# Kernel tuning notes

Measured on AMD Instinct MI355X. Metric: run time of the kernel, lower is better.

The kernel has to match this reference:

```python
import jax, jax.numpy as jnp
import numpy as np

H, FH, D = 8, 4, 64          # num_heads, focal_heads, att_size
HID = H * D                   # hidden_size = 512
B, S = 8, 512                 # batch, num_nodes
T_HOP, T_EDGE = 32, 16
SCALE = D ** -0.5


def setup_inputs() -> dict:
    key = jax.random.key(0)
    ks = jax.random.split(key, 24)
    f = lambda i, shape: jax.random.normal(ks[i], shape, jnp.float32)
    w = 1.0 / np.sqrt(HID)
    inp = {
        'q': f(0, (B, S, HID)), 'k': f(1, (B, S, HID)), 'v': f(2, (B, S, HID)),
        'query_hop_emb': f(3, (T_HOP, HID)) * 0.02,
        'query_edge_emb': f(4, (T_EDGE, HID)) * 0.02,
        'key_hop_emb': f(5, (T_HOP, HID)) * 0.02,
        'key_edge_emb': f(6, (T_EDGE, HID)) * 0.02,
        'value_hop_emb': f(7, (T_HOP, HID)) * 0.02,
        'value_edge_emb': f(8, (T_EDGE, HID)) * 0.02,
        'distance': jax.random.randint(ks[9], (B, S, S), 0, T_HOP),
        'edge_attr': jax.random.randint(ks[10], (B, S, S), 0, T_EDGE),
        # guarantee at least one unmasked key per query row to keep softmax finite
        'mask': jax.random.bernoulli(ks[11], 0.9, (B, S)).at[:, 0].set(True),
        'focal_mask': jax.random.bernoulli(ks[12], 0.5, (B, S, S)).at[:, :, 0].set(True),
        'Wq': f(13, (HID, H * D)) * w, 'bq': f(14, (H * D,)) * 0.01,
        'Wk': f(15, (HID, H * D)) * w, 'bk': f(16, (H * D,)) * 0.01,
        'Wv': f(17, (HID, H * D)) * w, 'bv': f(18, (H * D,)) * 0.01,
        'Wo': f(19, (H * D, HID)) * w, 'bo': f(20, (HID,)) * 0.01,
    }
    return inp


def _emb_scores(x, emb):
    # x: [B,H,S,D], emb: [T, H*D] -> per-head scores [B,H,S,T]
    e = emb.reshape(-1, H, D).transpose(1, 0, 2)  # [H,T,D]
    return jnp.einsum('bhsd,htd->bhst', x, e)


def _gather_last(scores, idx):
    # scores: [B,H,S,T], idx: [B,S,S] -> [B,H,S,S]
    idx_b = jnp.broadcast_to(idx[:, None], (B, H, S, S))
    return jnp.take_along_axis(scores, idx_b, axis=3)


def _scatter_add_last(attn, idx, T):
    # attn: [B,H,S,S], idx: [B,S,S] -> [B,H,S,T] accumulating attn weights
    idx_b = jnp.broadcast_to(idx[:, None], (B, H, S, S)).reshape(B * H * S, S)
    rows = jnp.arange(B * H * S)[:, None]
    flat = (rows * T + idx_b).reshape(-1)
    out = jnp.zeros((B * H * S * T,), attn.dtype).at[flat].add(attn.reshape(-1))
    return out.reshape(B, H, S, T)


def reference(q, k, v, query_hop_emb, query_edge_emb, key_hop_emb, key_edge_emb,
              value_hop_emb, value_edge_emb, distance, edge_attr, mask, focal_mask,
              Wq, bq, Wk, bk, Wv, bv, Wo, bo):
    qh = (q @ Wq + bq).reshape(B, S, H, D).transpose(0, 2, 1, 3)  # [B,H,S,D]
    kh = (k @ Wk + bk).reshape(B, S, H, D).transpose(0, 2, 1, 3)
    vh = (v @ Wv + bv).reshape(B, S, H, D).transpose(0, 2, 1, 3)

    spatial_bias = (_gather_last(_emb_scores(qh, query_hop_emb), distance)
                    + _gather_last(_emb_scores(kh, key_hop_emb), distance))
    edge_bias = (_gather_last(_emb_scores(qh, query_edge_emb), edge_attr)
                 + _gather_last(_emb_scores(kh, key_edge_emb), edge_attr))

    attn = (jnp.einsum('bhsd,bhtd->bhst', qh, kh) + spatial_bias + edge_bias) * SCALE

    GS = H - FH
    a1 = jnp.where(mask[:, None, None, :], attn[:, :GS], -jnp.inf)
    a2 = jnp.where(focal_mask[:, None], attn[:, GS:], -jnp.inf)
    attn = jax.nn.softmax(jnp.concatenate([a1, a2], axis=1), axis=3)

    vha = _scatter_add_last(attn, distance, T_HOP)   # [B,H,S,T_HOP]
    vea = _scatter_add_last(attn, edge_attr, T_EDGE)  # [B,H,S,T_EDGE]
    vh_emb = value_hop_emb.reshape(T_HOP, H, D).transpose(1, 0, 2)   # [H,T,D]
    ve_emb = value_edge_emb.reshape(T_EDGE, H, D).transpose(1, 0, 2)

    x = (jnp.einsum('bhst,bhtd->bhsd', attn, vh)
         + jnp.einsum('bhst,htd->bhsd', vha, vh_emb)
         + jnp.einsum('bhst,htd->bhsd', vea, ve_emb))
    x = x.transpose(0, 2, 1, 3).reshape(B, S, H * D)
    return x @ Wo + bo
```

## Files before the change

### kernel.cpp

```cpp
#include <hip/hip_runtime.h>

constexpr int nB = 8, nS = 512, nH = 8, nD = 64, nHID = 512;
constexpr int THOP = 32, TEDGE = 16;
constexpr float SCALE = 0.125f;
constexpr float NEGINF = -30000.0f;

typedef __attribute__((ext_vector_type(8))) short bf16x8;
typedef __attribute__((ext_vector_type(4))) float f32x4;

#define MFMA16(A, B, C) __builtin_amdgcn_mfma_f32_16x16x32_bf16(A, B, C, 0, 0, 0)

__device__ __align__(16) unsigned short g_qhi[(size_t)nB * nH * nS * nD];
__device__ __align__(16) unsigned short g_qlo[(size_t)nB * nH * nS * nD];
__device__ __align__(16) unsigned short g_khi[(size_t)nB * nH * nS * nD];
__device__ __align__(16) unsigned short g_klo[(size_t)nB * nH * nS * nD];
__device__ __align__(16) unsigned short g_vhiT[(size_t)nB * nH * nD * nS];
__device__ __align__(16) unsigned short g_vloT[(size_t)nB * nH * nD * nS];
__device__ __align__(16) unsigned short g_embh[96 * 512];
__device__ __align__(16) unsigned short g_embl[96 * 512];
__device__ __align__(16) unsigned short g_inhi[(size_t)3 * 2097152];
__device__ __align__(16) unsigned short g_inlo[(size_t)3 * 2097152];
__device__ __align__(16) unsigned short g_wth[(size_t)4 * 262144];
__device__ __align__(16) unsigned short g_wtl[(size_t)4 * 262144];
__device__ __align__(16) unsigned short g_xhi[(size_t)nB * nS * nHID];
__device__ __align__(16) unsigned short g_xlo[(size_t)nB * nS * nHID];
__device__ int g_flags[32];

__device__ __forceinline__ float ldf(const void* p, int isf32, size_t i) {
  if (isf32) return ((const float*)p)[i];
  unsigned int w = (unsigned int)(((const unsigned short*)p)[i]) << 16;
  return __uint_as_float(w);
}
__device__ __forceinline__ float bf2f(unsigned short h) {
  return __uint_as_float((unsigned)h << 16);
}
__device__ __forceinline__ float4 ldf4(const void* p, int isf32, size_t i) {
  if (isf32) return ((const float4*)p)[i >> 2];
  const ushort4 u = ((const ushort4*)p)[i >> 2];
  float4 r;
  r.x = bf2f(u.x); r.y = bf2f(u.y); r.z = bf2f(u.z); r.w = bf2f(u.w);
  return r;
}
__device__ __forceinline__ unsigned short f2bf(float x) {
  unsigned u = __float_as_uint(x);
  u += 0x7FFFu + ((u >> 16) & 1u);
  return (unsigned short)(u >> 16);
}

__device__ int detect_bool_mode(const unsigned char* p) {
  if (p[0] == 0x80 && p[1] == 0x3F) return 2;
  if (p[0] == 0x00 && p[1] == 0x3C) return 4;
  if (p[0] == 0x00 && p[3] == 0x3F) return 3;
  for (int i = 0; i < 64; i += 4)
    if (p[i + 1] | p[i + 2] | p[i + 3]) return 1;
  return 0;
}
__device__ __forceinline__ bool bool_at(const unsigned char* p, int mode, size_t i) {
  switch (mode) {
    case 0: return ((const int*)p)[i] != 0;
    case 1: return p[i] != 0;
    case 3: return ((const float*)p)[i] != 0.f;
    default: return ((const unsigned short*)p)[i] != 0;
  }
}

__global__ __launch_bounds__(256) void detect_all(
    const void* q, const void* k, const void* v,
    const void* qhe, const void* qee, const void* khe, const void* kee,
    const void* vhe, const void* vee,
    const int* dist, const int* edge,
    const unsigned char* mraw, const unsigned char* fraw,
    const void* Wq, const void* bq, const void* Wk, const void* bk,
    const void* Wv, const void* bv, const void* Wo, const void* bo) {
  __shared__ float sred[256];
  __shared__ int nzs;
  const int tid = threadIdx.x;
  const int blk = blockIdx.x;

  if (blk < 17) {
    const void* arrs[17] = {q, k, v, qhe, qee, khe, kee, vhe, vee,
                            Wq, bq, Wk, bk, Wv, bv, Wo, bo};
    const int full[17] = {2097152, 2097152, 2097152, 8192, 8192, 8192, 8192,
                          8192, 8192, 262144, 512, 262144, 512, 262144, 512,
                          262144, 512};
    const int n = full[blk] < 16384 ? full[blk] : 16384;
    const unsigned short* u = (const unsigned short*)arrs[blk];
    float m = 0.f;
    for (int i = tid; i < n; i += 256) {
      float x = __uint_as_float((unsigned int)u[i] << 16);
      if (x != x) x = 1e20f;
      m = fmaxf(m, fabsf(x));
    }
    sred[tid] = m;
    __syncthreads();
    for (int s = 128; s > 0; s >>= 1) {
      if (tid < s) sred[tid] = fmaxf(sred[tid], sred[tid + s]);
      __syncthreads();
    }
    if (tid == 0) g_flags[4 + blk] = (sred[0] > 1e3f) ? 1 : 0;
  } else if (blk == 17 || blk == 18) {
    const int* p = (blk == 17) ? dist : edge;
    if (tid == 0) nzs = 0;
    __syncthreads();
    int a = 0;
    for (int i = tid; i < 4096; i += 256) a |= p[2 * i + 1];
    if (a) atomicOr(&nzs, 1);
    __syncthreads();
    if (tid == 0) g_flags[blk - 17] = (nzs == 0);
  } else {
    if (tid == 0) {
      g_flags[2] = detect_bool_mode(mraw);
      g_flags[3] = detect_bool_mode(fraw);
    }
  }
}

__global__ __launch_bounds__(256) void emb_prep(
    const void* qhe, const void* khe, const void* qee, const void* kee) {
  const int blk = blockIdx.x;
  const void* srcs[4] = {qhe, khe, qee, kee};
  const int flagIdx[4] = {7, 9, 8, 10};
  const int counts[4] = {32 * 512, 32 * 512, 16 * 512, 16 * 512};
  const int dsts[4] = {0, 32 * 512, 64 * 512, 80 * 512};
  const int f = g_flags[flagIdx[blk]];
  const void* src = srcs[blk];
  const int n = counts[blk], d0 = dsts[blk];
  for (int i = threadIdx.x; i < n; i += 256) {
    const float x = ldf(src, f, i);
    const unsigned short hi = f2bf(x);
    g_embh[d0 + i] = hi;
    g_embl[d0 + i] = f2bf(x - bf2f(hi));
  }
}

__global__ __launch_bounds__(256) void split_prep(
    const void* q, const void* k, const void* v) {
  const int t = blockIdx.y;
  const void* srcs[3] = {q, k, v};
  const int f = g_flags[4 + t];
  const size_t base = (size_t)t * 2097152;
  const size_t i = ((size_t)blockIdx.x * 256 + threadIdx.x) * 4;
  const float4 v4 = ldf4(srcs[t], f, i);
  ushort4 h4, l4;
  h4.x = f2bf(v4.x); l4.x = f2bf(v4.x - bf2f(h4.x));
  h4.y = f2bf(v4.y); l4.y = f2bf(v4.y - bf2f(h4.y));
  h4.z = f2bf(v4.z); l4.z = f2bf(v4.z - bf2f(h4.z));
  h4.w = f2bf(v4.w); l4.w = f2bf(v4.w - bf2f(h4.w));
  *(ushort4*)&g_inhi[base + i] = h4;
  *(ushort4*)&g_inlo[base + i] = l4;
}

__global__ __launch_bounds__(256) void wt_prep(
    const void* Wq, const void* Wk, const void* Wv, const void* Wo) {
  __shared__ float t[64][65];
  const int mat = blockIdx.y;
  const void* srcs[4] = {Wq, Wk, Wv, Wo};
  const int fIdx[4] = {13, 15, 17, 19};
  const int f = g_flags[fIdx[mat]];
  const void* W = srcs[mat];
  const int k0 = (blockIdx.x >> 3) * 64, n0 = (blockIdx.x & 7) * 64;
  const int tid = threadIdx.x;
  const int r = tid >> 4, c4 = (tid & 15) * 4;
#pragma unroll
  for (int i = 0; i < 4; ++i) {
    const float4 v4 = ldf4(W, f, (size_t)(k0 + r + i * 16) * 512 + n0 + c4);
    t[r + i * 16][c4] = v4.x;
    t[r + i * 16][c4 + 1] = v4.y;
    t[r + i * 16][c4 + 2] = v4.z;
    t[r + i * 16][c4 + 3] = v4.w;
  }
  __syncthreads();
  unsigned short* dh = g_wth + (size_t)mat * 262144;
  unsigned short* dl = g_wtl + (size_t)mat * 262144;
#pragma unroll
  for (int i = 0; i < 4; ++i) {
    const int rn = r + i * 16;
    ushort4 h4, l4;
    const float v0 = t[c4][rn], v1 = t[c4 + 1][rn];
    const float v2 = t[c4 + 2][rn], v3 = t[c4 + 3][rn];
    h4.x = f2bf(v0); l4.x = f2bf(v0 - bf2f(h4.x));
    h4.y = f2bf(v1); l4.y = f2bf(v1 - bf2f(h4.y));
    h4.z = f2bf(v2); l4.z = f2bf(v2 - bf2f(h4.z));
    h4.w = f2bf(v3); l4.w = f2bf(v3 - bf2f(h4.w));
    *(ushort4*)&dh[(size_t)(n0 + rn) * 512 + k0 + c4] = h4;
    *(ushort4*)&dl[(size_t)(n0 + rn) * 512 + k0 + c4] = l4;
  }
}

template <int MODE_SEL>
__device__ __forceinline__ void gemm_body(
    const unsigned short* Ahi, const unsigned short* Alo,
    const unsigned short* Wth, const unsigned short* Wtl,
    const void* bias, int bF, float* dst, int mode, int m0, int n0) {
  __shared__ unsigned short As_hi[64][40];
  __shared__ unsigned short As_lo[64][40];
  __shared__ unsigned short Wt_hi[64][40];
  __shared__ unsigned short Wt_lo[64][40];
  const int tid = threadIdx.x;
  const int w = tid >> 6, l = tid & 63, c = l & 15, g = l >> 4;
  const int wr = w >> 1, wc = w & 1;
  const int sr = tid >> 2, sc = (tid & 3) * 8;

  f32x4 acc[2][2] = {{{0.f, 0.f, 0.f, 0.f}, {0.f, 0.f, 0.f, 0.f}},
                     {{0.f, 0.f, 0.f, 0.f}, {0.f, 0.f, 0.f, 0.f}}};

  const size_t ga = (size_t)(m0 + sr) * 512 + sc;
  const size_t gw = (size_t)(n0 + sr) * 512 + sc;
  bf16x8 pa_h = *(const bf16x8*)(Ahi + ga);
  bf16x8 pa_l = *(const bf16x8*)(Alo + ga);
  bf16x8 pw_h = *(const bf16x8*)(Wth + gw);
  bf16x8 pw_l = *(const bf16x8*)(Wtl + gw);

  for (int k0 = 0; k0 < 512; k0 += 32) {
    __syncthreads();
    *(bf16x8*)&As_hi[sr][sc] = pa_h;
    *(bf16x8*)&As_lo[sr][sc] = pa_l;
    *(bf16x8*)&Wt_hi[sr][sc] = pw_h;
    *(bf16x8*)&Wt_lo[sr][sc] = pw_l;
    __syncthreads();
    if (k0 < 480) {
      pa_h = *(const bf16x8*)(Ahi + ga + k0 + 32);
      pa_l = *(const bf16x8*)(Alo + ga + k0 + 32);
      pw_h = *(const bf16x8*)(Wth + gw + k0 + 32);
      pw_l = *(const bf16x8*)(Wtl + gw + k0 + 32);
    }
#pragma unroll
    for (int mi = 0; mi < 2; ++mi) {
      const bf16x8 ah = *(const bf16x8*)&As_hi[wr * 32 + mi * 16 + c][g * 8];
      const bf16x8 al = *(const bf16x8*)&As_lo[wr * 32 + mi * 16 + c][g * 8];
#pragma unroll
      for (int nj = 0; nj < 2; ++nj) {
        const bf16x8 wh = *(const bf16x8*)&Wt_hi[wc * 32 + nj * 16 + c][g * 8];
        const bf16x8 wl = *(const bf16x8*)&Wt_lo[wc * 32 + nj * 16 + c][g * 8];
        acc[mi][nj] = MFMA16(ah, wh, acc[mi][nj]);
        acc[mi][nj] = MFMA16(al, wh, acc[mi][nj]);
        acc[mi][nj] = MFMA16(ah, wl, acc[mi][nj]);
      }
    }
  }
#pragma unroll
  for (int mi = 0; mi < 2; ++mi)
#pragma unroll
    for (int nj = 0; nj < 2; ++nj)
#pragma unroll
      for (int r = 0; r < 4; ++r) {
        const int m = m0 + wr * 32 + mi * 16 + 4 * g + r;
        const int n = n0 + wc * 32 + nj * 16 + c;
        const float v2 = acc[mi][nj][r] + ldf(bias, bF, n);
        if (MODE_SEL == 3) {
          dst[(size_t)m * 512 + n] = v2;
        } else {
          const int b = m >> 9, s = m & 511, h = n >> 6, d = n & 63;
          const unsigned short hi = f2bf(v2);
          const unsigned short lo = f2bf(v2 - bf2f(hi));
          if (mode == 0) {
            const size_t i0 = (((size_t)(b * nH + h) * nS) + s) * nD + d;
            g_qhi[i0] = hi; g_qlo[i0] = lo;
          } else if (mode == 1) {
            const size_t i0 = (((size_t)(b * nH + h) * nS) + s) * nD + d;
            g_khi[i0] = hi; g_klo[i0] = lo;
          } else {
            const size_t i0 = (((size_t)(b * nH + h) * nD) + d) * nS + s;
            g_vhiT[i0] = hi; g_vloT[i0] = lo;
          }
        }
      }
}

__global__ __launch_bounds__(256, 4) void gemm_qkv(
    const unsigned short* __restrict__ inhi, const unsigned short* __restrict__ inlo,
    const unsigned short* __restrict__ wth, const unsigned short* __restrict__ wtl,
    const void* __restrict__ bq, const void* __restrict__ bk,
    const void* __restrict__ bv) {
  const int mat = blockIdx.y >> 6;
  const int m0 = (blockIdx.y & 63) * 64, n0 = blockIdx.x * 64;
  const void* bias = (mat == 0) ? bq : (mat == 1) ? bk : bv;
  const int bF = g_flags[14 + 2 * mat];
  gemm_body<0>(inhi + (size_t)mat * 2097152, inlo + (size_t)mat * 2097152,
               wth + (size_t)mat * 262144, wtl + (size_t)mat * 262144,
               bias, bF, nullptr, mat, m0, n0);
}

__global__ __launch_bounds__(256, 4) void gemm_out(
    const unsigned short* __restrict__ Ahi, const unsigned short* __restrict__ Alo,
    const unsigned short* __restrict__ Wth, const unsigned short* __restrict__ Wtl,
    const void* __restrict__ bias, float* __restrict__ dst) {
  gemm_body<3>(Ahi, Alo, Wth, Wtl, bias, g_flags[20], dst, 3,
               blockIdx.y * 64, blockIdx.x * 64);
}

__global__ __launch_bounds__(256, 3) void attn_kernel(
    const int* __restrict__ dist, const int* __restrict__ edge,
    const unsigned char* __restrict__ mraw, const unsigned char* __restrict__ fraw,
    const void* __restrict__ vhe, const void* __restrict__ vee) {
  __shared__ unsigned short kvbuf[8192];
  __shared__ unsigned short plds[16][536];
  __shared__ float x_s[64][17];
  __shared__ float chop_s[16][33];
  __shared__ float cedge_s[16][17];
  __shared__ float vha_s[16][33];
  __shared__ float vea_s[16][17];
  __shared__ float red_s[16][4];
  __shared__ float red2_s[16][4];
  __shared__ float rinv_s[16];

  const int id = blockIdx.x;
  const int bh = (id & 7) * 8 + ((id >> 3) & 7);
  const int qt = id >> 6;
  const int b = bh >> 3, h = bh & 7;
  const int q0 = qt * 16;
  const int tid = threadIdx.x;
  const int w = tid >> 6, l = tid & 63, c = l & 15, g = l >> 4;

  const int d64 = g_flags[0], e64 = g_flags[1];
  const int mmode = g_flags[2], fmode = g_flags[3];
  const int fvhe = g_flags[11], fvee = g_flags[12];

  for (int i = tid; i < 16 * 33; i += 256) (&vha_s[0][0])[i] = 0.f;
  for (int i = tid; i < 16 * 17; i += 256) (&vea_s[0][0])[i] = 0.f;
  for (int i = tid; i < 64 * 17; i += 256) (&x_s[0][0])[i] = 0.f;

  const int e0 = tid << 3;
  const int kr0 = e0 >> 6, kd0 = e0 & 63;
  const int vd0 = e0 >> 7, vcol = e0 & 127;
  bf16x8 rkh0, rkh1;
  bf16x8 rv0, rv1, rv2, rv3;

  auto loadKhi = [&](int ch) {
    const size_t base = ((size_t)bh * nS + ch * 64) * nD + kd0;
    rkh0 = *(const bf16x8*)(g_khi + base + (size_t)kr0 * nD);
    rkh1 = *(const bf16x8*)(g_khi + base + (size_t)(kr0 + 32) * nD);
  };
  auto writeKhi = [&](int buf) {
    const int base = buf * 4096;
    const int dst0 = (kr0 << 6) + (((kd0 >> 3) ^ (kr0 & 7)) << 3);
    const int dst1 = ((kr0 + 32) << 6) + (((kd0 >> 3) ^ ((kr0 + 32) & 7)) << 3);
    *(bf16x8*)&kvbuf[base + dst0] = rkh0;
    *(bf16x8*)&kvbuf[base + dst1] = rkh1;
  };
  auto loadV = [&](int p) {
    const size_t base = (size_t)bh * nD * nS + (p << 7) + vcol;
    rv0 = *(const bf16x8*)(g_vhiT + base + (size_t)vd0 * nS);
    rv1 = *(const bf16x8*)(g_vhiT + base + (size_t)(vd0 + 16) * nS);
    rv2 = *(const bf16x8*)(g_vhiT + base + (size_t)(vd0 + 32) * nS);
    rv3 = *(const bf16x8*)(g_vhiT + base + (size_t)(vd0 + 48) * nS);
  };
  auto writeV = [&]() {
    const int swz = ((vcol >> 3) ^ (vd0 & 15)) << 3;
    *(bf16x8*)&kvbuf[(vd0 << 7) + swz] = rv0;
    *(bf16x8*)&kvbuf[((vd0 + 16) << 7) + swz] = rv1;
    *(bf16x8*)&kvbuf[((vd0 + 32) << 7) + swz] = rv2;
    *(bf16x8*)&kvbuf[((vd0 + 48) << 7) + swz] = rv3;
  };

  loadKhi(0);

  const size_t rowbase = ((size_t)b * nS + q0) * nS;
  for (int j4 = tid; j4 < 2048; j4 += 256) {
    const int j = j4 * 4, r = j >> 9, c1 = j & 511;
    int dv[4], ev[4];
    if (!d64) {
      const int4 t = ((const int4*)(dist + rowbase))[j4];
      dv[0] = t.x & 31; dv[1] = t.y & 31; dv[2] = t.z & 31; dv[3] = t.w & 31;
    } else {
      const int4 t0 = ((const int4*)(dist + 2 * rowbase))[2 * j4];
      const int4 t1 = ((const int4*)(dist + 2 * rowbase))[2 * j4 + 1];
      dv[0] = t0.x & 31; dv[1] = t0.z & 31; dv[2] = t1.x & 31; dv[3] = t1.z & 31;
    }
    if (!e64) {
      const int4 t = ((const int4*)(edge + rowbase))[j4];
      ev[0] = t.x & 15; ev[1] = t.y & 15; ev[2] = t.z & 15; ev[3] = t.w & 15;
    } else {
      const int4 t0 = ((const int4*)(edge + 2 * rowbase))[2 * j4];
      const int4 t1 = ((const int4*)(edge + 2 * rowbase))[2 * j4 + 1];
      ev[0] = t0.x & 15; ev[1] = t0.z & 15; ev[2] = t1.x & 15; ev[3] = t1.z & 15;
    }
    ushort4 pw;
    unsigned short* pp = (unsigned short*)&pw;
#pragma unroll
    for (int t = 0; t < 4; ++t) {
      const bool keep = (h < 4) ? bool_at(mraw, mmode, (size_t)b * nS + c1 + t)
                                : bool_at(fraw, fmode, rowbase + j + t);
      pp[t] = (unsigned short)(dv[t] | (ev[t] << 5) | ((int)keep << 9));
    }
    *(ushort4*)&plds[r][c1] = pw;
  }

  const size_t qbase = (((size_t)bh * nS) + q0 + c) * nD + g * 8;
  const bf16x8 qh0 = *(const bf16x8*)(g_qhi + qbase);
  const bf16x8 qh1 = *(const bf16x8*)(g_qhi + qbase + 32);
  const bf16x8 ql0 = *(const bf16x8*)(g_qlo + qbase);
  const bf16x8 ql1 = *(const bf16x8*)(g_qlo + qbase + 32);

  if (w < 3) {
    const bool isEdge = (w == 2);
    const int tb = (w == 1) ? 16 : 0;
    const size_t qe0 = (isEdge ? (size_t)64 * 512 : 0) + (size_t)(tb + c) * 512 + h * 64;
    const size_t ke0 = (isEdge ? (size_t)80 * 512 : (size_t)32 * 512) + (size_t)(tb + c) * 512 + h * 64;
    f32x4 acc = {0.f, 0.f, 0.f, 0.f};
#pragma unroll
    for (int dh = 0; dh < 2; ++dh) {
      const bf16x8 qhh = dh ? qh1 : qh0;
      const bf16x8 qll = dh ? ql1 : ql0;
      const bf16x8 khq = *(const bf16x8*)(g_khi + qbase + dh * 32);
      const bf16x8 klq = *(const bf16x8*)(g_klo + qbase + dh * 32);
      const bf16x8 eqh = *(const bf16x8*)(g_embh + qe0 + dh * 32 + g * 8);
      const bf16x8 eql = *(const bf16x8*)(g_embl + qe0 + dh * 32 + g * 8);
      const bf16x8 ekh = *(const bf16x8*)(g_embh + ke0 + dh * 32 + g * 8);
      const bf16x8 ekl = *(const bf16x8*)(g_embl + ke0 + dh * 32 + g * 8);
      acc = MFMA16(qhh, eqh, acc);
      acc = MFMA16(qll, eqh, acc);
      acc = MFMA16(qhh, eql, acc);
      acc = MFMA16(khq, ekh, acc);
      acc = MFMA16(klq, ekh, acc);
      acc = MFMA16(khq, ekl, acc);
    }
    if (!isEdge) {
#pragma unroll
      for (int r = 0; r < 4; ++r) chop_s[4 * g + r][tb + c] = acc[r];
    } else {
#pragma unroll
      for (int r = 0; r < 4; ++r) cedge_s[4 * g + r][c] = acc[r];
    }
  }

  writeKhi(0);
  __syncthreads();

  f32x4 pS[8];
  const int sw8 = c & 7;
  const int krow = w * 16 + c;
  for (int ch = 0; ch < 8; ++ch) {
    if (ch < 7) loadKhi(ch + 1);
    const unsigned short* kb_ = kvbuf + (ch & 1) * 4096;
    const size_t klbase = ((size_t)bh * nS + ch * 64 + krow) * nD + g * 8;
    const bf16x8 kl0 = *(const bf16x8*)(g_klo + klbase);
    const bf16x8 kl1 = *(const bf16x8*)(g_klo + klbase + 32);
    const int a0 = krow << 6;
    const bf16x8 kh0 = *(const bf16x8*)&kb_[a0 + ((g ^ sw8) << 3)];
    const bf16x8 kh1 = *(const bf16x8*)&kb_[a0 + (((4 + g) ^ sw8) << 3)];
    f32x4 acc = {0.f, 0.f, 0.f, 0.f};
    __builtin_amdgcn_s_setprio(1);
    acc = MFMA16(kh0, qh0, acc);
    acc = MFMA16(kh0, ql0, acc);
    acc = MFMA16(kh1, qh1, acc);
    acc = MFMA16(kh1, ql1, acc);
    acc = MFMA16(kl0, qh0, acc);
    acc = MFMA16(kl1, qh1, acc);
    __builtin_amdgcn_s_setprio(0);
    const int key0 = ch * 64 + w * 16 + 4 * g;
    const ushort4 pv4 = *(const ushort4*)&plds[c][key0];
    const unsigned short pp[4] = {pv4.x, pv4.y, pv4.z, pv4.w};
#pragma unroll
    for (int r = 0; r < 4; ++r) {
      const float s = (acc[r] + chop_s[c][pp[r] & 31] +
                       cedge_s[c][(pp[r] >> 5) & 15]) * SCALE;
      pS[ch][r] = (pp[r] & 512) ? s : NEGINF;
    }
    if (ch < 7) {
      writeKhi((ch + 1) & 1);
      __syncthreads();
    }
  }

  loadV(0);

  float mx = NEGINF;
#pragma unroll
  for (int kt = 0; kt < 8; ++kt)
#pragma unroll
    for (int r = 0; r < 4; ++r) mx = fmaxf(mx, pS[kt][r]);
  mx = fmaxf(mx, __shfl_xor(mx, 16));
  mx = fmaxf(mx, __shfl_xor(mx, 32));
  if (l < 16) red_s[c][w] = mx;
  __syncthreads();
  const float M = fmaxf(fmaxf(red_s[c][0], red_s[c][1]),
                        fmaxf(red_s[c][2], red_s[c][3]));
  float sum = 0.f;
#pragma unroll
  for (int kt = 0; kt < 8; ++kt) {
    const int key0 = kt * 64 + w * 16 + 4 * g;
    const ushort4 pv4 = *(const ushort4*)&plds[c][key0];
    const unsigned short pp[4] = {pv4.x, pv4.y, pv4.z, pv4.w};
    float pv[4];
#pragma unroll
    for (int r = 0; r < 4; ++r) {
      pv[r] = __expf(pS[kt][r] - M);
      sum += pv[r];
      atomicAdd(&vha_s[c][pp[r] & 31], pv[r]);
      atomicAdd(&vea_s[c][(pp[r] >> 5) & 15], pv[r]);
    }
    *(unsigned*)&plds[c][key0] =
        ((unsigned)f2bf(pv[1]) << 16) | (unsigned)f2bf(pv[0]);
    *(unsigned*)&plds[c][key0 + 2] =
        ((unsigned)f2bf(pv[3]) << 16) | (unsigned)f2bf(pv[2]);
  }
  sum += __shfl_xor(sum, 16);
  sum += __shfl_xor(sum, 32);
  if (l < 16) red2_s[c][w] = sum;
  writeV();
  __syncthreads();
  if (w == 0 && l < 16) {
    const float tot = red2_s[c][0] + red2_s[c][1] + red2_s[c][2] + red2_s[c][3];
    rinv_s[c] = 1.0f / tot;
  }

  f32x4 oacc[4] = {{0.f, 0.f, 0.f, 0.f}, {0.f, 0.f, 0.f, 0.f},
                   {0.f, 0.f, 0.f, 0.f}, {0.f, 0.f, 0.f, 0.f}};
  for (int p = 0; p < 4; ++p) {
    if (p < 3) loadV(p + 1);
    const int col16 = (w << 1) + (g & 1) + ((g >> 1) << 3);
    const int j0 = (p << 7) + ((g >> 1) << 6) + (w << 4) + ((g & 1) << 3);
    const bf16x8 bu = *(const bf16x8*)&plds[c][j0];
    __builtin_amdgcn_s_setprio(1);
#pragma unroll
    for (int t = 0; t < 4; ++t) {
      const int row = t * 16 + c;
      const bf16x8 vh_ = *(const bf16x8*)&kvbuf[(row << 7) + ((col16 ^ c) << 3)];
      const bf16x8 vl_ = *(const bf16x8*)(g_vloT + (((size_t)bh * nD) + row) * nS + j0);
      oacc[t] = MFMA16(vh_, bu, oacc[t]);
      oacc[t] = MFMA16(vl_, bu, oacc[t]);
    }
    __builtin_amdgcn_s_setprio(0);
    if (p < 3) {
      __syncthreads();
      writeV();
      __syncthreads();
    }
  }
#pragma unroll
  for (int t = 0; t < 4; ++t)
#pragma unroll
    for (int r = 0; r < 4; ++r)
      atomicAdd(&x_s[t * 16 + 4 * g + r][c], oacc[t][r]);
  __syncthreads();

  {
    const int d = tid & 63, qq = tid >> 6;
    float val[4];
#pragma unroll
    for (int j = 0; j < 4; ++j) val[j] = x_s[d][qq + 4 * j];
    for (int t = 0; t < THOP; ++t) {
      const float e = ldf(vhe, fvhe, (size_t)t * nHID + h * 64 + d);
#pragma unroll
      for (int j = 0; j < 4; ++j) val[j] += vha_s[qq + 4 * j][t] * e;
    }
    for (int t = 0; t < TEDGE; ++t) {
      const float e = ldf(vee, fvee, (size_t)t * nHID + h * 64 + d);
#pragma unroll
      for (int j = 0; j < 4; ++j) val[j] += vea_s[qq + 4 * j][t] * e;
    }
#pragma unroll
    for (int j = 0; j < 4; ++j) {
      const int q = qq + 4 * j;
      const float xv = val[j] * rinv_s[q];
      const unsigned short hi = f2bf(xv);
      const size_t i0 = ((size_t)b * nS + q0 + q) * nHID + h * 64 + d;
      g_xhi[i0] = hi;
      g_xlo[i0] = f2bf(xv - bf2f(hi));
    }
  }
}

extern "C" void kernel_launch(void* const* d_in, const int* in_sizes, int n_in,
                              void* d_out, int out_size, void* d_ws, size_t ws_size,
                              hipStream_t stream) {
  const void* q   = d_in[0];
  const void* k   = d_in[1];
  const void* v   = d_in[2];
  const void* qhe = d_in[3];
  const void* qee = d_in[4];
  const void* khe = d_in[5];
  const void* kee = d_in[6];
  const void* vhe = d_in[7];
  const void* vee = d_in[8];
  const int* dist = (const int*)d_in[9];
  const int* edge = (const int*)d_in[10];
  const unsigned char* mraw = (const unsigned char*)d_in[11];
  const unsigned char* fraw = (const unsigned char*)d_in[12];
  const void* Wq = d_in[13];
  const void* bq = d_in[14];
  const void* Wk = d_in[15];
  const void* bk = d_in[16];
  const void* Wv = d_in[17];
  const void* bv = d_in[18];
  const void* Wo = d_in[19];
  const void* bo = d_in[20];

  detect_all<<<20, 256, 0, stream>>>(q, k, v, qhe, qee, khe, kee, vhe, vee,
                                     dist, edge, mraw, fraw,
                                     Wq, bq, Wk, bk, Wv, bv, Wo, bo);
  emb_prep<<<4, 256, 0, stream>>>(qhe, khe, qee, kee);
  split_prep<<<dim3(2048, 3), 256, 0, stream>>>(q, k, v);
  wt_prep<<<dim3(64, 4), 256, 0, stream>>>(Wq, Wk, Wv, Wo);

  unsigned short* inhi; hipGetSymbolAddress((void**)&inhi, HIP_SYMBOL(g_inhi));
  unsigned short* inlo; hipGetSymbolAddress((void**)&inlo, HIP_SYMBOL(g_inlo));
  unsigned short* wth;  hipGetSymbolAddress((void**)&wth,  HIP_SYMBOL(g_wth));
  unsigned short* wtl;  hipGetSymbolAddress((void**)&wtl,  HIP_SYMBOL(g_wtl));
  unsigned short* xhi;  hipGetSymbolAddress((void**)&xhi,  HIP_SYMBOL(g_xhi));
  unsigned short* xlo;  hipGetSymbolAddress((void**)&xlo,  HIP_SYMBOL(g_xlo));

  gemm_qkv<<<dim3(8, 192), 256, 0, stream>>>(inhi, inlo, wth, wtl, bq, bk, bv);
  attn_kernel<<<2048, 256, 0, stream>>>(dist, edge, mraw, fraw, vhe, vee);
  gemm_out<<<dim3(8, 64), 256, 0, stream>>>(xhi, xlo,
                                            wth + 3 * 262144, wtl + 3 * 262144,
                                            bo, (float*)d_out);
}
```

Baseline: 587.2 us.

## Split fused attention kernel into separate QK-softmax and PV kernels via global staging

```diff
diff --git a/kernel.cpp b/kernel.cpp
--- a/kernel.cpp
+++ b/kernel.cpp
@@ -24,6 +24,8 @@
 __device__ __align__(16) unsigned short g_wtl[(size_t)4 * 262144];
 __device__ __align__(16) unsigned short g_xhi[(size_t)nB * nS * nHID];
 __device__ __align__(16) unsigned short g_xlo[(size_t)nB * nS * nHID];
+__device__ __align__(16) unsigned short g_P[(size_t)2048 * 16 * 512];
+__device__ float g_aux[(size_t)2048 * 784];
 __device__ int g_flags[32];
 
 __device__ __forceinline__ float ldf(const void* p, int isf32, size_t i) {
@@ -289,20 +291,17 @@
                blockIdx.y * 64, blockIdx.x * 64);
 }
 
-__global__ __launch_bounds__(256, 3) void attn_kernel(
+__global__ __launch_bounds__(256, 3) void attn_qk(
     const int* __restrict__ dist, const int* __restrict__ edge,
-    const unsigned char* __restrict__ mraw, const unsigned char* __restrict__ fraw,
-    const void* __restrict__ vhe, const void* __restrict__ vee) {
+    const unsigned char* __restrict__ mraw, const unsigned char* __restrict__ fraw) {
   __shared__ unsigned short kvbuf[8192];
   __shared__ unsigned short plds[16][536];
-  __shared__ float x_s[64][17];
   __shared__ float chop_s[16][33];
   __shared__ float cedge_s[16][17];
   __shared__ float vha_s[16][33];
   __shared__ float vea_s[16][17];
   __shared__ float red_s[16][4];
   __shared__ float red2_s[16][4];
-  __shared__ float rinv_s[16];
 
   const int id = blockIdx.x;
   const int bh = (id & 7) * 8 + ((id >> 3) & 7);
@@ -314,17 +313,13 @@
 
   const int d64 = g_flags[0], e64 = g_flags[1];
   const int mmode = g_flags[2], fmode = g_flags[3];
-  const int fvhe = g_flags[11], fvee = g_flags[12];
 
   for (int i = tid; i < 16 * 33; i += 256) (&vha_s[0][0])[i] = 0.f;
   for (int i = tid; i < 16 * 17; i += 256) (&vea_s[0][0])[i] = 0.f;
-  for (int i = tid; i < 64 * 17; i += 256) (&x_s[0][0])[i] = 0.f;
 
   const int e0 = tid << 3;
   const int kr0 = e0 >> 6, kd0 = e0 & 63;
-  const int vd0 = e0 >> 7, vcol = e0 & 127;
   bf16x8 rkh0, rkh1;
-  bf16x8 rv0, rv1, rv2, rv3;
 
   auto loadKhi = [&](int ch) {
     const size_t base = ((size_t)bh * nS + ch * 64) * nD + kd0;
@@ -337,20 +332,6 @@
     const int dst1 = ((kr0 + 32) << 6) + (((kd0 >> 3) ^ ((kr0 + 32) & 7)) << 3);
     *(bf16x8*)&kvbuf[base + dst0] = rkh0;
     *(bf16x8*)&kvbuf[base + dst1] = rkh1;
-  };
-  auto loadV = [&](int p) {
-    const size_t base = (size_t)bh * nD * nS + (p << 7) + vcol;
-    rv0 = *(const bf16x8*)(g_vhiT + base + (size_t)vd0 * nS);
-    rv1 = *(const bf16x8*)(g_vhiT + base + (size_t)(vd0 + 16) * nS);
-    rv2 = *(const bf16x8*)(g_vhiT + base + (size_t)(vd0 + 32) * nS);
-    rv3 = *(const bf16x8*)(g_vhiT + base + (size_t)(vd0 + 48) * nS);
-  };
-  auto writeV = [&]() {
-    const int swz = ((vcol >> 3) ^ (vd0 & 15)) << 3;
-    *(bf16x8*)&kvbuf[(vd0 << 7) + swz] = rv0;
-    *(bf16x8*)&kvbuf[((vd0 + 16) << 7) + swz] = rv1;
-    *(bf16x8*)&kvbuf[((vd0 + 32) << 7) + swz] = rv2;
-    *(bf16x8*)&kvbuf[((vd0 + 48) << 7) + swz] = rv3;
   };
 
   loadKhi(0);
@@ -463,8 +444,6 @@
     }
   }
 
-  loadV(0);
-
   float mx = NEGINF;
 #pragma unroll
   for (int kt = 0; kt < 8; ++kt)
@@ -498,25 +477,88 @@
   sum += __shfl_xor(sum, 16);
   sum += __shfl_xor(sum, 32);
   if (l < 16) red2_s[c][w] = sum;
+  __syncthreads();
+
+  for (int i = tid; i < 1024; i += 256) {
+    const int row = i >> 6, col = (i & 63) << 3;
+    *(bf16x8*)&g_P[((size_t)id * 16 + row) * 512 + col] =
+        *(const bf16x8*)&plds[row][col];
+  }
+  float* aux = g_aux + (size_t)id * 784;
+  for (int i = tid; i < 512; i += 256) aux[i] = vha_s[i >> 5][i & 31];
+  if (tid < 256) aux[512 + tid] = vea_s[tid >> 4][tid & 15];
+  if (w == 0 && l < 16) {
+    const float tot = red2_s[c][0] + red2_s[c][1] + red2_s[c][2] + red2_s[c][3];
+    aux[768 + c] = 1.0f / tot;
+  }
+}
+
+__global__ __launch_bounds__(256, 4) void attn_pv(
+    const void* __restrict__ vhe, const void* __restrict__ vee) {
+  __shared__ unsigned short vbuf[8192];
+  __shared__ float vha_s[16][33];
+  __shared__ float vea_s[16][17];
+  __shared__ float rinv_s[16];
+  __shared__ float x_s[64][17];
+
+  const int id = blockIdx.x;
+  const int bh = (id & 7) * 8 + ((id >> 3) & 7);
+  const int qt = id >> 6;
+  const int b = bh >> 3, h = bh & 7;
+  const int q0 = qt * 16;
+  const int tid = threadIdx.x;
+  const int w = tid >> 6, l = tid & 63, c = l & 15, g = l >> 4;
+  const int fvhe = g_flags[11], fvee = g_flags[12];
+
+  const int e0 = tid << 3;
+  const int vd0 = e0 >> 7, vcol = e0 & 127;
+  bf16x8 rv0, rv1, rv2, rv3;
+
+  auto loadV = [&](int p) {
+    const size_t base = (size_t)bh * nD * nS + (p << 7) + vcol;
+    rv0 = *(const bf16x8*)(g_vhiT + base + (size_t)vd0 * nS);
+    rv1 = *(const bf16x8*)(g_vhiT + base + (size_t)(vd0 + 16) * nS);
+    rv2 = *(const bf16x8*)(g_vhiT + base + (size_t)(vd0 + 32) * nS);
+    rv3 = *(const bf16x8*)(g_vhiT + base + (size_t)(vd0 + 48) * nS);
+  };
+  auto writeV = [&]() {
+    const int swz = ((vcol >> 3) ^ (vd0 & 15)) << 3;
+    *(bf16x8*)&vbuf[(vd0 << 7) + swz] = rv0;
+    *(bf16x8*)&vbuf[((vd0 + 16) << 7) + swz] = rv1;
+    *(bf16x8*)&vbuf[((vd0 + 32) << 7) + swz] = rv2;
+    *(bf16x8*)&vbuf[((vd0 + 48) << 7) + swz] = rv3;
+  };
+
+  loadV(0);
+
+  const float* aux = g_aux + (size_t)id * 784;
+  for (int i = tid; i < 512; i += 256) vha_s[i >> 5][i & 31] = aux[i];
+  if (tid < 256) vea_s[tid >> 4][tid & 15] = aux[512 + tid];
+  if (tid < 16) rinv_s[tid] = aux[768 + tid];
+  for (int i = tid; i < 64 * 17; i += 256) (&x_s[0][0])[i] = 0.f;
+
+  const int jbase = ((g >> 1) << 6) + (w << 4) + ((g & 1) << 3);
+  const size_t pbase = ((size_t)id * 16 + c) * 512 + jbase;
+  bf16x8 bu = *(const bf16x8*)(g_P + pbase);
+  const int col16 = (w << 1) + (g & 1) + ((g >> 1) << 3);
+
   writeV();
   __syncthreads();
-  if (w == 0 && l < 16) {
-    const float tot = red2_s[c][0] + red2_s[c][1] + red2_s[c][2] + red2_s[c][3];
-    rinv_s[c] = 1.0f / tot;
-  }
 
   f32x4 oacc[4] = {{0.f, 0.f, 0.f, 0.f}, {0.f, 0.f, 0.f, 0.f},
                    {0.f, 0.f, 0.f, 0.f}, {0.f, 0.f, 0.f, 0.f}};
   for (int p = 0; p < 4; ++p) {
-    if (p < 3) loadV(p + 1);
-    const int col16 = (w << 1) + (g & 1) + ((g >> 1) << 3);
-    const int j0 = (p << 7) + ((g >> 1) << 6) + (w << 4) + ((g & 1) << 3);
-    const bf16x8 bu = *(const bf16x8*)&plds[c][j0];
+    bf16x8 bunext;
+    if (p < 3) {
+      loadV(p + 1);
+      bunext = *(const bf16x8*)(g_P + pbase + (p + 1) * 128);
+    }
+    const int j0 = jbase + p * 128;
     __builtin_amdgcn_s_setprio(1);
 #pragma unroll
     for (int t = 0; t < 4; ++t) {
       const int row = t * 16 + c;
-      const bf16x8 vh_ = *(const bf16x8*)&kvbuf[(row << 7) + ((col16 ^ c) << 3)];
+      const bf16x8 vh_ = *(const bf16x8*)&vbuf[(row << 7) + ((col16 ^ c) << 3)];
       const bf16x8 vl_ = *(const bf16x8*)(g_vloT + (((size_t)bh * nD) + row) * nS + j0);
       oacc[t] = MFMA16(vh_, bu, oacc[t]);
       oacc[t] = MFMA16(vl_, bu, oacc[t]);
@@ -526,6 +568,7 @@
       __syncthreads();
       writeV();
       __syncthreads();
+      bu = bunext;
     }
   }
 #pragma unroll
@@ -540,11 +583,13 @@
     float val[4];
 #pragma unroll
     for (int j = 0; j < 4; ++j) val[j] = x_s[d][qq + 4 * j];
+#pragma unroll
     for (int t = 0; t < THOP; ++t) {
       const float e = ldf(vhe, fvhe, (size_t)t * nHID + h * 64 + d);
 #pragma unroll
       for (int j = 0; j < 4; ++j) val[j] += vha_s[qq + 4 * j][t] * e;
     }
+#pragma unroll
     for (int t = 0; t < TEDGE; ++t) {
       const float e = ldf(vee, fvee, (size_t)t * nHID + h * 64 + d);
 #pragma unroll
@@ -602,7 +647,8 @@
   unsigned short* xlo;  hipGetSymbolAddress((void**)&xlo,  HIP_SYMBOL(g_xlo));
 
   gemm_qkv<<<dim3(8, 192), 256, 0, stream>>>(inhi, inlo, wth, wtl, bq, bk, bv);
-  attn_kernel<<<2048, 256, 0, stream>>>(dist, edge, mraw, fraw, vhe, vee);
+  attn_qk<<<2048, 256, 0, stream>>>(dist, edge, mraw, fraw);
+  attn_pv<<<2048, 256, 0, stream>>>(vhe, vee);
   gemm_out<<<dim3(8, 64), 256, 0, stream>>>(xhi, xlo,
                                             wth + 3 * 262144, wtl + 3 * 262144,
                                             bo, (float*)d_out);
```

Result: slower. 638.9 us (+8.8%).

## Process 32 query rows per attention block to reuse K/V tiles

Applied to the files above, without the earlier changes.

```diff
diff --git a/kernel.cpp b/kernel.cpp
--- a/kernel.cpp
+++ b/kernel.cpp
@@ -289,26 +289,26 @@
                blockIdx.y * 64, blockIdx.x * 64);
 }
 
-__global__ __launch_bounds__(256, 3) void attn_kernel(
+__global__ __launch_bounds__(256, 2) void attn_kernel(
     const int* __restrict__ dist, const int* __restrict__ edge,
     const unsigned char* __restrict__ mraw, const unsigned char* __restrict__ fraw,
     const void* __restrict__ vhe, const void* __restrict__ vee) {
   __shared__ unsigned short kvbuf[8192];
-  __shared__ unsigned short plds[16][536];
-  __shared__ float x_s[64][17];
-  __shared__ float chop_s[16][33];
-  __shared__ float cedge_s[16][17];
-  __shared__ float vha_s[16][33];
-  __shared__ float vea_s[16][17];
-  __shared__ float red_s[16][4];
-  __shared__ float red2_s[16][4];
-  __shared__ float rinv_s[16];
+  __shared__ unsigned short plds[32][520];
+  __shared__ float x_s[64][33];
+  __shared__ float chop_s[32][33];
+  __shared__ float cedge_s[32][17];
+  __shared__ float vha_s[32][33];
+  __shared__ float vea_s[32][17];
+  __shared__ float red_s[32][4];
+  __shared__ float red2_s[32][4];
+  __shared__ float rinv_s[32];
 
   const int id = blockIdx.x;
   const int bh = (id & 7) * 8 + ((id >> 3) & 7);
   const int qt = id >> 6;
   const int b = bh >> 3, h = bh & 7;
-  const int q0 = qt * 16;
+  const int q0 = qt * 32;
   const int tid = threadIdx.x;
   const int w = tid >> 6, l = tid & 63, c = l & 15, g = l >> 4;
 
@@ -316,9 +316,9 @@
   const int mmode = g_flags[2], fmode = g_flags[3];
   const int fvhe = g_flags[11], fvee = g_flags[12];
 
-  for (int i = tid; i < 16 * 33; i += 256) (&vha_s[0][0])[i] = 0.f;
-  for (int i = tid; i < 16 * 17; i += 256) (&vea_s[0][0])[i] = 0.f;
-  for (int i = tid; i < 64 * 17; i += 256) (&x_s[0][0])[i] = 0.f;
+  for (int i = tid; i < 32 * 33; i += 256) (&vha_s[0][0])[i] = 0.f;
+  for (int i = tid; i < 32 * 17; i += 256) (&vea_s[0][0])[i] = 0.f;
+  for (int i = tid; i < 64 * 33; i += 256) (&x_s[0][0])[i] = 0.f;
 
   const int e0 = tid << 3;
   const int kr0 = e0 >> 6, kd0 = e0 & 63;
@@ -356,7 +356,7 @@
   loadKhi(0);
 
   const size_t rowbase = ((size_t)b * nS + q0) * nS;
-  for (int j4 = tid; j4 < 2048; j4 += 256) {
+  for (int j4 = tid; j4 < 4096; j4 += 256) {
     const int j = j4 * 4, r = j >> 9, c1 = j & 511;
     int dv[4], ev[4];
     if (!d64) {
@@ -386,48 +386,64 @@
     *(ushort4*)&plds[r][c1] = pw;
   }
 
-  const size_t qbase = (((size_t)bh * nS) + q0 + c) * nD + g * 8;
-  const bf16x8 qh0 = *(const bf16x8*)(g_qhi + qbase);
-  const bf16x8 qh1 = *(const bf16x8*)(g_qhi + qbase + 32);
-  const bf16x8 ql0 = *(const bf16x8*)(g_qlo + qbase);
-  const bf16x8 ql1 = *(const bf16x8*)(g_qlo + qbase + 32);
-
-  if (w < 3) {
-    const bool isEdge = (w == 2);
-    const int tb = (w == 1) ? 16 : 0;
-    const size_t qe0 = (isEdge ? (size_t)64 * 512 : 0) + (size_t)(tb + c) * 512 + h * 64;
-    const size_t ke0 = (isEdge ? (size_t)80 * 512 : (size_t)32 * 512) + (size_t)(tb + c) * 512 + h * 64;
-    f32x4 acc = {0.f, 0.f, 0.f, 0.f};
-#pragma unroll
-    for (int dh = 0; dh < 2; ++dh) {
-      const bf16x8 qhh = dh ? qh1 : qh0;
-      const bf16x8 qll = dh ? ql1 : ql0;
-      const bf16x8 khq = *(const bf16x8*)(g_khi + qbase + dh * 32);
-      const bf16x8 klq = *(const bf16x8*)(g_klo + qbase + dh * 32);
-      const bf16x8 eqh = *(const bf16x8*)(g_embh + qe0 + dh * 32 + g * 8);
-      const bf16x8 eql = *(const bf16x8*)(g_embl + qe0 + dh * 32 + g * 8);
-      const bf16x8 ekh = *(const bf16x8*)(g_embh + ke0 + dh * 32 + g * 8);
-      const bf16x8 ekl = *(const bf16x8*)(g_embl + ke0 + dh * 32 + g * 8);
-      acc = MFMA16(qhh, eqh, acc);
-      acc = MFMA16(qll, eqh, acc);
-      acc = MFMA16(qhh, eql, acc);
-      acc = MFMA16(khq, ekh, acc);
-      acc = MFMA16(klq, ekh, acc);
-      acc = MFMA16(khq, ekl, acc);
-    }
-    if (!isEdge) {
-#pragma unroll
-      for (int r = 0; r < 4; ++r) chop_s[4 * g + r][tb + c] = acc[r];
-    } else {
-#pragma unroll
-      for (int r = 0; r < 4; ++r) cedge_s[4 * g + r][c] = acc[r];
+  const size_t qbaseA = (((size_t)bh * nS) + q0 + c) * nD + g * 8;
+  const size_t qbaseB = qbaseA + 16 * nD;
+  const bf16x8 qh0a = *(const bf16x8*)(g_qhi + qbaseA);
+  const bf16x8 qh1a = *(const bf16x8*)(g_qhi + qbaseA + 32);
+  const bf16x8 ql0a = *(const bf16x8*)(g_qlo + qbaseA);
+  const bf16x8 ql1a = *(const bf16x8*)(g_qlo + qbaseA + 32);
+  const bf16x8 qh0b = *(const bf16x8*)(g_qhi + qbaseB);
+  const bf16x8 qh1b = *(const bf16x8*)(g_qhi + qbaseB + 32);
+  const bf16x8 ql0b = *(const bf16x8*)(g_qlo + qbaseB);
+  const bf16x8 ql1b = *(const bf16x8*)(g_qlo + qbaseB + 32);
+
+#pragma unroll
+  for (int it = 0; it < 2; ++it) {
+    const int task = w + 4 * it;
+    if (task < 6) {
+      const int half = task / 3;
+      const int sub = task - half * 3;
+      const bool isEdge = (sub == 2);
+      const int tb = (sub == 1) ? 16 : 0;
+      const size_t qb_ = half ? qbaseB : qbaseA;
+      const bf16x8 qh0_ = half ? qh0b : qh0a;
+      const bf16x8 qh1_ = half ? qh1b : qh1a;
+      const bf16x8 ql0_ = half ? ql0b : ql0a;
+      const bf16x8 ql1_ = half ? ql1b : ql1a;
+      const size_t qe0 = (isEdge ? (size_t)64 * 512 : 0) + (size_t)(tb + c) * 512 + h * 64;
+      const size_t ke0 = (isEdge ? (size_t)80 * 512 : (size_t)32 * 512) + (size_t)(tb + c) * 512 + h * 64;
+      f32x4 acc = {0.f, 0.f, 0.f, 0.f};
+#pragma unroll
+      for (int dh = 0; dh < 2; ++dh) {
+        const bf16x8 qhh = dh ? qh1_ : qh0_;
+        const bf16x8 qll = dh ? ql1_ : ql0_;
+        const bf16x8 khq = *(const bf16x8*)(g_khi + qb_ + dh * 32);
+        const bf16x8 klq = *(const bf16x8*)(g_klo + qb_ + dh * 32);
+        const bf16x8 eqh = *(const bf16x8*)(g_embh + qe0 + dh * 32 + g * 8);
+        const bf16x8 eql = *(const bf16x8*)(g_embl + qe0 + dh * 32 + g * 8);
+        const bf16x8 ekh = *(const bf16x8*)(g_embh + ke0 + dh * 32 + g * 8);
+        const bf16x8 ekl = *(const bf16x8*)(g_embl + ke0 + dh * 32 + g * 8);
+        acc = MFMA16(qhh, eqh, acc);
+        acc = MFMA16(qll, eqh, acc);
+        acc = MFMA16(qhh, eql, acc);
+        acc = MFMA16(khq, ekh, acc);
+        acc = MFMA16(klq, ekh, acc);
+        acc = MFMA16(khq, ekl, acc);
+      }
+      if (!isEdge) {
+#pragma unroll
+        for (int r = 0; r < 4; ++r) chop_s[half * 16 + 4 * g + r][tb + c] = acc[r];
+      } else {
+#pragma unroll
+        for (int r = 0; r < 4; ++r) cedge_s[half * 16 + 4 * g + r][c] = acc[r];
+      }
     }
   }
 
   writeKhi(0);
   __syncthreads();
 
-  f32x4 pS[8];
+  f32x4 pSa[8], pSb[8];
   const int sw8 = c & 7;
   const int krow = w * 16 + c;
   for (int ch = 0; ch < 8; ++ch) {
@@ -439,23 +455,35 @@
     const int a0 = krow << 6;
     const bf16x8 kh0 = *(const bf16x8*)&kb_[a0 + ((g ^ sw8) << 3)];
     const bf16x8 kh1 = *(const bf16x8*)&kb_[a0 + (((4 + g) ^ sw8) << 3)];
-    f32x4 acc = {0.f, 0.f, 0.f, 0.f};
+    f32x4 acca = {0.f, 0.f, 0.f, 0.f};
+    f32x4 accb = {0.f, 0.f, 0.f, 0.f};
     __builtin_amdgcn_s_setprio(1);
-    acc = MFMA16(kh0, qh0, acc);
-    acc = MFMA16(kh0, ql0, acc);
-    acc = MFMA16(kh1, qh1, acc);
-    acc = MFMA16(kh1, ql1, acc);
-    acc = MFMA16(kl0, qh0, acc);
-    acc = MFMA16(kl1, qh1, acc);
+    acca = MFMA16(kh0, qh0a, acca);
+    accb = MFMA16(kh0, qh0b, accb);
+    acca = MFMA16(kh0, ql0a, acca);
+    accb = MFMA16(kh0, ql0b, accb);
+    acca = MFMA16(kh1, qh1a, acca);
+    accb = MFMA16(kh1, qh1b, accb);
+    acca = MFMA16(kh1, ql1a, acca);
+    accb = MFMA16(kh1, ql1b, accb);
+    acca = MFMA16(kl0, qh0a, acca);
+    accb = MFMA16(kl0, qh0b, accb);
+    acca = MFMA16(kl1, qh1a, acca);
+    accb = MFMA16(kl1, qh1b, accb);
     __builtin_amdgcn_s_setprio(0);
     const int key0 = ch * 64 + w * 16 + 4 * g;
-    const ushort4 pv4 = *(const ushort4*)&plds[c][key0];
-    const unsigned short pp[4] = {pv4.x, pv4.y, pv4.z, pv4.w};
+    const ushort4 pa4 = *(const ushort4*)&plds[c][key0];
+    const ushort4 pb4 = *(const ushort4*)&plds[16 + c][key0];
+    const unsigned short ppa[4] = {pa4.x, pa4.y, pa4.z, pa4.w};
+    const unsigned short ppb[4] = {pb4.x, pb4.y, pb4.z, pb4.w};
 #pragma unroll
     for (int r = 0; r < 4; ++r) {
-      const float s = (acc[r] + chop_s[c][pp[r] & 31] +
-                       cedge_s[c][(pp[r] >> 5) & 15]) * SCALE;
-      pS[ch][r] = (pp[r] & 512) ? s : NEGINF;
+      const float sa = (acca[r] + chop_s[c][ppa[r] & 31] +
+                        cedge_s[c][(ppa[r] >> 5) & 15]) * SCALE;
+      pSa[ch][r] = (ppa[r] & 512) ? sa : NEGINF;
+      const float sb = (accb[r] + chop_s[16 + c][ppb[r] & 31] +
+                        cedge_s[16 + c][(ppb[r] >> 5) & 15]) * SCALE;
+      pSb[ch][r] = (ppb[r] & 512) ? sb : NEGINF;
     }
     if (ch < 7) {
       writeKhi((ch + 1) & 1);
@@ -463,63 +491,87 @@
     }
   }
 
-  loadV(0);
-
-  float mx = NEGINF;
+  float mxa = NEGINF, mxb = NEGINF;
 #pragma unroll
   for (int kt = 0; kt < 8; ++kt)
 #pragma unroll
-    for (int r = 0; r < 4; ++r) mx = fmaxf(mx, pS[kt][r]);
-  mx = fmaxf(mx, __shfl_xor(mx, 16));
-  mx = fmaxf(mx, __shfl_xor(mx, 32));
-  if (l < 16) red_s[c][w] = mx;
+    for (int r = 0; r < 4; ++r) {
+      mxa = fmaxf(mxa, pSa[kt][r]);
+      mxb = fmaxf(mxb, pSb[kt][r]);
+    }
+  mxa = fmaxf(mxa, __shfl_xor(mxa, 16));
+  mxa = fmaxf(mxa, __shfl_xor(mxa, 32));
+  mxb = fmaxf(mxb, __shfl_xor(mxb, 16));
+  mxb = fmaxf(mxb, __shfl_xor(mxb, 32));
+  if (l < 16) { red_s[c][w] = mxa; red_s[16 + c][w] = mxb; }
   __syncthreads();
-  const float M = fmaxf(fmaxf(red_s[c][0], red_s[c][1]),
-                        fmaxf(red_s[c][2], red_s[c][3]));
-  float sum = 0.f;
+  const float Ma = fmaxf(fmaxf(red_s[c][0], red_s[c][1]),
+                         fmaxf(red_s[c][2], red_s[c][3]));
+  const float Mb = fmaxf(fmaxf(red_s[16 + c][0], red_s[16 + c][1]),
+                         fmaxf(red_s[16 + c][2], red_s[16 + c][3]));
+  float suma = 0.f, sumb = 0.f;
 #pragma unroll
   for (int kt = 0; kt < 8; ++kt) {
     const int key0 = kt * 64 + w * 16 + 4 * g;
-    const ushort4 pv4 = *(const ushort4*)&plds[c][key0];
-    const unsigned short pp[4] = {pv4.x, pv4.y, pv4.z, pv4.w};
-    float pv[4];
+    const ushort4 pa4 = *(const ushort4*)&plds[c][key0];
+    const ushort4 pb4 = *(const ushort4*)&plds[16 + c][key0];
+    const unsigned short ppa[4] = {pa4.x, pa4.y, pa4.z, pa4.w};
+    const unsigned short ppb[4] = {pb4.x, pb4.y, pb4.z, pb4.w};
+    float pva[4], pvb[4];
 #pragma unroll
     for (int r = 0; r < 4; ++r) {
-      pv[r] = __expf(pS[kt][r] - M);
-      sum += pv[r];
-      atomicAdd(&vha_s[c][pp[r] & 31], pv[r]);
-      atomicAdd(&vea_s[c][(pp[r] >> 5) & 15], pv[r]);
+      pva[r] = __expf(pSa[kt][r] - Ma);
+      suma += pva[r];
+      atomicAdd(&vha_s[c][ppa[r] & 31], pva[r]);
+      atomicAdd(&vea_s[c][(ppa[r] >> 5) & 15], pva[r]);
+      pvb[r] = __expf(pSb[kt][r] - Mb);
+      sumb += pvb[r];
+      atomicAdd(&vha_s[16 + c][ppb[r] & 31], pvb[r]);
+      atomicAdd(&vea_s[16 + c][(ppb[r] >> 5) & 15], pvb[r]);
     }
     *(unsigned*)&plds[c][key0] =
-        ((unsigned)f2bf(pv[1]) << 16) | (unsigned)f2bf(pv[0]);
+        ((unsigned)f2bf(pva[1]) << 16) | (unsigned)f2bf(pva[0]);
     *(unsigned*)&plds[c][key0 + 2] =
-        ((unsigned)f2bf(pv[3]) << 16) | (unsigned)f2bf(pv[2]);
-  }
-  sum += __shfl_xor(sum, 16);
-  sum += __shfl_xor(sum, 32);
-  if (l < 16) red2_s[c][w] = sum;
+        ((unsigned)f2bf(pva[3]) << 16) | (unsigned)f2bf(pva[2]);
+    *(unsigned*)&plds[16 + c][key0] =
+        ((unsigned)f2bf(pvb[1]) << 16) | (unsigned)f2bf(pvb[0]);
+    *(unsigned*)&plds[16 + c][key0 + 2] =
+        ((unsigned)f2bf(pvb[3]) << 16) | (unsigned)f2bf(pvb[2]);
+  }
+  suma += __shfl_xor(suma, 16);
+  suma += __shfl_xor(suma, 32);
+  sumb += __shfl_xor(sumb, 16);
+  sumb += __shfl_xor(sumb, 32);
+  if (l < 16) { red2_s[c][w] = suma; red2_s[16 + c][w] = sumb; }
+  loadV(0);
   writeV();
   __syncthreads();
   if (w == 0 && l < 16) {
-    const float tot = red2_s[c][0] + red2_s[c][1] + red2_s[c][2] + red2_s[c][3];
-    rinv_s[c] = 1.0f / tot;
-  }
-
-  f32x4 oacc[4] = {{0.f, 0.f, 0.f, 0.f}, {0.f, 0.f, 0.f, 0.f},
-                   {0.f, 0.f, 0.f, 0.f}, {0.f, 0.f, 0.f, 0.f}};
+    rinv_s[c] = 1.0f / (red2_s[c][0] + red2_s[c][1] + red2_s[c][2] + red2_s[c][3]);
+    rinv_s[16 + c] = 1.0f / (red2_s[16 + c][0] + red2_s[16 + c][1] +
+                             red2_s[16 + c][2] + red2_s[16 + c][3]);
+  }
+
+  f32x4 oacca[4] = {{0.f, 0.f, 0.f, 0.f}, {0.f, 0.f, 0.f, 0.f},
+                    {0.f, 0.f, 0.f, 0.f}, {0.f, 0.f, 0.f, 0.f}};
+  f32x4 oaccb[4] = {{0.f, 0.f, 0.f, 0.f}, {0.f, 0.f, 0.f, 0.f},
+                    {0.f, 0.f, 0.f, 0.f}, {0.f, 0.f, 0.f, 0.f}};
   for (int p = 0; p < 4; ++p) {
     if (p < 3) loadV(p + 1);
     const int col16 = (w << 1) + (g & 1) + ((g >> 1) << 3);
     const int j0 = (p << 7) + ((g >> 1) << 6) + (w << 4) + ((g & 1) << 3);
-    const bf16x8 bu = *(const bf16x8*)&plds[c][j0];
+    const bf16x8 bua = *(const bf16x8*)&plds[c][j0];
+    const bf16x8 bub = *(const bf16x8*)&plds[16 + c][j0];
     __builtin_amdgcn_s_setprio(1);
 #pragma unroll
     for (int t = 0; t < 4; ++t) {
       const int row = t * 16 + c;
       const bf16x8 vh_ = *(const bf16x8*)&kvbuf[(row << 7) + ((col16 ^ c) << 3)];
       const bf16x8 vl_ = *(const bf16x8*)(g_vloT + (((size_t)bh * nD) + row) * nS + j0);
-      oacc[t] = MFMA16(vh_, bu, oacc[t]);
-      oacc[t] = MFMA16(vl_, bu, oacc[t]);
+      oacca[t] = MFMA16(vh_, bua, oacca[t]);
+      oaccb[t] = MFMA16(vh_, bub, oaccb[t]);
+      oacca[t] = MFMA16(vl_, bua, oacca[t]);
+      oaccb[t] = MFMA16(vl_, bub, oaccb[t]);
     }
     __builtin_amdgcn_s_setprio(0);
     if (p < 3) {
@@ -531,27 +583,31 @@
 #pragma unroll
   for (int t = 0; t < 4; ++t)
 #pragma unroll
-    for (int r = 0; r < 4; ++r)
-      atomicAdd(&x_s[t * 16 + 4 * g + r][c], oacc[t][r]);
+    for (int r = 0; r < 4; ++r) {
+      atomicAdd(&x_s[t * 16 + 4 * g + r][c], oacca[t][r]);
+      atomicAdd(&x_s[t * 16 + 4 * g + r][16 + c], oaccb[t][r]);
+    }
   __syncthreads();
 
   {
     const int d = tid & 63, qq = tid >> 6;
-    float val[4];
-#pragma unroll
-    for (int j = 0; j < 4; ++j) val[j] = x_s[d][qq + 4 * j];
+    float val[8];
+#pragma unroll
+    for (int j = 0; j < 8; ++j) val[j] = x_s[d][qq + 4 * j];
+#pragma unroll
     for (int t = 0; t < THOP; ++t) {
       const float e = ldf(vhe, fvhe, (size_t)t * nHID + h * 64 + d);
 #pragma unroll
-      for (int j = 0; j < 4; ++j) val[j] += vha_s[qq + 4 * j][t] * e;
-    }
+      for (int j = 0; j < 8; ++j) val[j] += vha_s[qq + 4 * j][t] * e;
+    }
+#pragma unroll
     for (int t = 0; t < TEDGE; ++t) {
       const float e = ldf(vee, fvee, (size_t)t * nHID + h * 64 + d);
 #pragma unroll
-      for (int j = 0; j < 4; ++j) val[j] += vea_s[qq + 4 * j][t] * e;
-    }
-#pragma unroll
-    for (int j = 0; j < 4; ++j) {
+      for (int j = 0; j < 8; ++j) val[j] += vea_s[qq + 4 * j][t] * e;
+    }
+#pragma unroll
+    for (int j = 0; j < 8; ++j) {
       const int q = qq + 4 * j;
       const float xv = val[j] * rinv_s[q];
       const unsigned short hi = f2bf(xv);
@@ -602,7 +658,7 @@
   unsigned short* xlo;  hipGetSymbolAddress((void**)&xlo,  HIP_SYMBOL(g_xlo));
 
   gemm_qkv<<<dim3(8, 192), 256, 0, stream>>>(inhi, inlo, wth, wtl, bq, bk, bv);
-  attn_kernel<<<2048, 256, 0, stream>>>(dist, edge, mraw, fraw, vhe, vee);
+  attn_kernel<<<1024, 256, 0, stream>>>(dist, edge, mraw, fraw, vhe, vee);
   gemm_out<<<dim3(8, 64), 256, 0, stream>>>(xhi, xlo,
                                             wth + 3 * 262144, wtl + 3 * 262144,
                                             bo, (float*)d_out);
```

Result: slower. 610.6 us (+4.0%).
